# Kernel tuning notes

Measured on AMD Instinct MI355X. Metric: run time of the kernel, lower is better.

## Reference

```python
import jax, jax.numpy as jnp
import numpy as np

# Module constants (match init_kwargs / DCNv4 defaults)
N, C, H, W = 4, 256, 128, 128
G = 4                       # DCNv4 default group
KS = 3                      # kernel_size
K = KS * KS                 # 9 sampling points per group
Cg = C // G                 # channels per group
PAD_OFF = int(np.ceil(G * K * 3 / 8) * 8)  # 112, padded offset_mask dim
EPS = 1e-5                  # BatchNorm2d eps


def setup_inputs() -> dict:
    key = jax.random.key(0)
    ks = jax.random.split(key, 6)
    s = 0.05
    return {
        "x": jax.random.normal(ks[0], (N, C, H, W), jnp.float32),
        "conv_w": jax.random.normal(ks[1], (C, C, 1, 1), jnp.float32) * s,
        "bn1_gamma": jnp.ones((C,), jnp.float32),
        "bn1_beta": jnp.zeros((C,), jnp.float32),
        "bn1_mean": jnp.zeros((C,), jnp.float32),
        "bn1_var": jnp.ones((C,), jnp.float32),
        "value_w": jax.random.normal(ks[2], (C, C), jnp.float32) * s,
        "value_b": jnp.zeros((C,), jnp.float32),
        "offset_w": jax.random.normal(ks[3], (PAD_OFF, C), jnp.float32) * s,
        "offset_b": jnp.zeros((PAD_OFF,), jnp.float32),
        "out_w": jax.random.normal(ks[4], (C, C), jnp.float32) * s,
        "out_b": jnp.zeros((C,), jnp.float32),
        "bn2_gamma": jnp.ones((C,), jnp.float32),
        "bn2_beta": jnp.zeros((C,), jnp.float32),
        "bn2_mean": jnp.zeros((C,), jnp.float32),
        "bn2_var": jnp.ones((C,), jnp.float32),
    }


def _bilinear(v, lh, lw):
    """Bilinear sample v:(N,H,W,G,Cg) at float locs lh/lw:(N,H,W,G); zero outside."""
    n, h, w, g, c = v.shape
    h0 = jnp.floor(lh)
    w0 = jnp.floor(lw)
    dh = lh - h0
    dw = lw - w0
    h0i = h0.astype(jnp.int32)
    w0i = w0.astype(jnp.int32)
    vf = v.reshape(n, h * w, g, c)

    def gather(hh, ww):
        valid = (hh >= 0) & (hh < h) & (ww >= 0) & (ww < w)
        idx = jnp.clip(hh, 0, h - 1) * w + jnp.clip(ww, 0, w - 1)
        out = jnp.take_along_axis(vf, idx.reshape(n, h * w, g)[..., None], axis=1)
        return out.reshape(n, h, w, g, c) * valid[..., None].astype(v.dtype)

    w00 = (1 - dh) * (1 - dw)
    w01 = (1 - dh) * dw
    w10 = dh * (1 - dw)
    w11 = dh * dw
    return (gather(h0i, w0i) * w00[..., None]
            + gather(h0i, w0i + 1) * w01[..., None]
            + gather(h0i + 1, w0i) * w10[..., None]
            + gather(h0i + 1, w0i + 1) * w11[..., None])


def _bn(x_nchw, gamma, beta, mean, var):
    scale = (gamma / jnp.sqrt(var + EPS))[None, :, None, None]
    return x_nchw * scale + (beta - mean * gamma / jnp.sqrt(var + EPS))[None, :, None, None]


def reference(x, conv_w, bn1_gamma, bn1_beta, bn1_mean, bn1_var,
              value_w, value_b, offset_w, offset_b, out_w, out_b,
              bn2_gamma, bn2_beta, bn2_mean, bn2_var):
    n, _, h, w = x.shape
    # ---- Conv(c1,c2,k=1): 1x1 conv (no bias) + BN + SiLU ----
    y = jnp.einsum('nchw,oc->nohw', x, conv_w[:, :, 0, 0])
    y = jax.nn.silu(_bn(y, bn1_gamma, bn1_beta, bn1_mean, bn1_var))

    # ---- DCNv4 on (N, L, C) tokens ----
    t = y.transpose(0, 2, 3, 1)                      # (N,H,W,C)
    v = t @ value_w.T + value_b                      # value_proj
    om = t @ offset_w.T + offset_b                   # (N,H,W,112)
    om = om[..., : G * K * 3].reshape(n, h, w, G, K * 3)
    off = om[..., : 2 * K].reshape(n, h, w, G, K, 2) # (dx, dy) per point
    mask = om[..., 2 * K:]                           # (N,H,W,G,K), no softmax in v4
    v = v.reshape(n, h, w, G, Cg)

    hi = jnp.arange(h, dtype=jnp.float32)[None, :, None, None]
    wi = jnp.arange(w, dtype=jnp.float32)[None, None, :, None]
    out = jnp.zeros_like(v)
    for k in range(K):  # fixed small kernel loop (9 points)
        i, j = divmod(k, KS)
        lh = hi + (i - 1) + off[..., k, 1]           # stride=1, pad=1, dil=1
        lw = wi + (j - 1) + off[..., k, 0]           # offset_scale=1.0
        out = out + mask[..., k, None] * _bilinear(v, lh, lw)

    o = out.reshape(n, h, w, C) @ out_w.T + out_b    # output_proj
    o = o.transpose(0, 3, 1, 2)                      # back to NCHW

    # ---- final BN + SiLU ----
    return jax.nn.silu(_bn(o, bn2_gamma, bn2_beta, bn2_mean, bn2_var))
```

## Files before the change

kernel.cpp:

```cpp
#include <hip/hip_runtime.h>
#include <cstdint>

typedef unsigned short u16;
typedef unsigned int   u32;
typedef __attribute__((ext_vector_type(8))) __bf16 bf16x8;
typedef __attribute__((ext_vector_type(2))) float  f32x2;
typedef __attribute__((ext_vector_type(4))) float  f32x4;
typedef __attribute__((ext_vector_type(4))) u32    u32x4;

#define N_IMG 4
#define C_DIM 256
#define H_DIM 128
#define W_DIM 128
#define HW    (H_DIM * W_DIM)
#define M_TOT (N_IMG * HW)
#define CG    64
#define PADOFF 112
#define NCAT  368
#define EPSV  1e-5f

__device__ __forceinline__ u16 f2b(float f) {
  u32 u = __float_as_uint(f);
  u += 0x7fffu + ((u >> 16) & 1u);
  return (u16)(u >> 16);
}

__device__ __forceinline__ void async_cp16(const void* g, void* l) {
  __builtin_amdgcn_global_load_lds(
      (const __attribute__((address_space(1))) void*)g,
      (__attribute__((address_space(3))) void*)l, 16, 0, 0);
}

__global__ __launch_bounds__(256) void cast_all(
    const float* __restrict__ a0, u16* __restrict__ o0,
    const float* __restrict__ a1, u16* __restrict__ o1,
    const float* __restrict__ a2, u16* __restrict__ o2,
    const float* __restrict__ a3, u16* __restrict__ o3) {
  int i = blockIdx.x * 256 + threadIdx.x;
  const float* in; u16* out; int base;
  if (i < 16384)      { in = a0; out = o0; base = 0; }
  else if (i < 32768) { in = a1; out = o1; base = 16384; }
  else if (i < 39936) { in = a2; out = o2; base = 32768; }
  else                { in = a3; out = o3; base = 39936; }
  int j = i - base;
  f32x4 v = reinterpret_cast<const f32x4*>(in)[j];
  u32 lo = (u32)f2b(v[0]) | ((u32)f2b(v[1]) << 16);
  u32 hi = (u32)f2b(v[2]) | ((u32)f2b(v[3]) << 16);
  reinterpret_cast<u32*>(out)[2 * j]     = lo;
  reinterpret_cast<u32*>(out)[2 * j + 1] = hi;
}

__global__ __launch_bounds__(256, 2) void fused_proj(
    const float* __restrict__ X, const u16* __restrict__ Bc,
    const u16* __restrict__ Wcat,
    u16* __restrict__ Vv, float* __restrict__ Om,
    const float* __restrict__ vbias, const float* __restrict__ obias,
    const float* __restrict__ gamma, const float* __restrict__ beta,
    const float* __restrict__ mean, const float* __restrict__ var) {
  constexpr int BM = 128, BK = 32;
  __shared__ __align__(16) u16 T[BM * C_DIM];
  __shared__ __align__(16) u16 As[BM * BK];
  __shared__ __align__(16) u16 Bs[BM * BK];
  const int tid  = threadIdx.x;
  const int lane = tid & 63;
  const int wave = tid >> 6;
  const int quad = lane >> 4;
  const int l16  = lane & 15;
  const int bm = blockIdx.x * BM;
  const int wm = (wave & 1) * 64;
  const int wn = (wave >> 1) * 64;
  const int img = bm >> 14;
  const int hw0 = bm & (HW - 1);
  const int p2  = (tid & 63) * 2;
  const int hh  = tid >> 6;
  const float* xb = X + (size_t)img * C_DIM * HW + hw0 + p2;

  f32x4 acc0[4][4] = {};
  f32x4 acc1[4][4] = {};
  for (int ko = 0; ko < C_DIM; ko += BK) {
    float a0[8], a1[8];
#pragma unroll
    for (int j = 0; j < 8; ++j) {
      f32x2 fv = *reinterpret_cast<const f32x2*>(
          xb + (size_t)(ko + hh * 8 + j) * HW);
      a0[j] = fv.x; a1[j] = fv.y;
    }
    u32x4 w0, w1;
#pragma unroll
    for (int j = 0; j < 4; ++j) {
      w0[j] = (u32)f2b(a0[2 * j]) | ((u32)f2b(a0[2 * j + 1]) << 16);
      w1[j] = (u32)f2b(a1[2 * j]) | ((u32)f2b(a1[2 * j + 1]) << 16);
    }
    {
      u32x4* Ar = reinterpret_cast<u32x4*>(As);
      int sw = hh ^ ((p2 >> 1) & 3);
      Ar[p2 * 4 + sw]       = w0;
      Ar[(p2 + 1) * 4 + sw] = w1;
    }
#pragma unroll
    for (int it = 0; it < 2; ++it) {
      int chunk = it * 256 + tid;
      int r  = chunk >> 2;
      int kk = (chunk & 3) << 3;
      async_cp16(Bc + (size_t)r * C_DIM + (ko + kk),
                 Bs + (size_t)(it * 256 + wave * 64) * 8);
    }
    __syncthreads();
    const bf16x8* Apf = reinterpret_cast<const bf16x8*>(As);
    const bf16x8* Bpf = reinterpret_cast<const bf16x8*>(Bs);
    bf16x8 af[4];
#pragma unroll
    for (int mi = 0; mi < 4; ++mi) {
      int r = wm + mi * 16 + l16;
      af[mi] = Apf[r * 4 + (quad ^ ((r >> 1) & 3))];
    }
    {
      bf16x8 bfr[4];
#pragma unroll
      for (int ni = 0; ni < 4; ++ni)
        bfr[ni] = Bpf[(wn + ni * 16 + l16) * 4 + quad];
#pragma unroll
      for (int mi = 0; mi < 4; ++mi)
#pragma unroll
        for (int ni = 0; ni < 4; ++ni)
          acc0[mi][ni] = __builtin_amdgcn_mfma_f32_16x16x32_bf16(
              af[mi], bfr[ni], acc0[mi][ni], 0, 0, 0);
    }
    __syncthreads();
#pragma unroll
    for (int it = 0; it < 2; ++it) {
      int chunk = it * 256 + tid;
      int r  = chunk >> 2;
      int kk = (chunk & 3) << 3;
      async_cp16(Bc + (size_t)(128 + r) * C_DIM + (ko + kk),
                 Bs + (size_t)(it * 256 + wave * 64) * 8);
    }
    __syncthreads();
    {
      bf16x8 bfr[4];
#pragma unroll
      for (int ni = 0; ni < 4; ++ni)
        bfr[ni] = Bpf[(wn + ni * 16 + l16) * 4 + quad];
#pragma unroll
      for (int mi = 0; mi < 4; ++mi)
#pragma unroll
        for (int ni = 0; ni < 4; ++ni)
          acc1[mi][ni] = __builtin_amdgcn_mfma_f32_16x16x32_bf16(
              af[mi], bfr[ni], acc1[mi][ni], 0, 0, 0);
    }
    __syncthreads();
  }
  auto epi1 = [&](f32x4 (&acc)[4][4], int bn) {
#pragma unroll
    for (int ni = 0; ni < 4; ++ni) {
      int n = bn + wn + ni * 16 + l16;
      float sc = gamma[n] * rsqrtf(var[n] + EPSV);
      float sh = beta[n] - mean[n] * sc;
#pragma unroll
      for (int mi = 0; mi < 4; ++mi) {
        int row = wm + mi * 16 + quad * 4;
#pragma unroll
        for (int i = 0; i < 4; ++i) {
          float y = acc[mi][ni][i] * sc + sh;
          y = y / (1.f + __expf(-y));
          int rr = row + i;
          T[rr * C_DIM + (((n >> 3) ^ (rr & 15)) << 3) + (n & 7)] = f2b(y);
        }
      }
    }
  };
  epi1(acc0, 0);
  epi1(acc1, 128);
  __syncthreads();

  auto stage2 = [&](u16* buf, int n0, int ko) {
#pragma unroll
    for (int it = 0; it < 2; ++it) {
      int chunk = it * 256 + tid;
      int r  = chunk >> 2;
      int kk = (chunk & 3) << 3;
      int br = n0 + r; if (br >= NCAT) br = NCAT - 1;
      async_cp16(Wcat + (size_t)br * C_DIM + (ko + kk),
                 buf + (size_t)(it * 256 + wave * 64) * 8);
    }
  };
  for (int nc = 0; nc < 3; ++nc) {
    const int n0 = nc * 128;
    f32x4 acc[4][4] = {};
    stage2(As, n0, 0);
    for (int koi = 0; koi < 8; ++koi) {
      const u16* cur = (koi & 1) ? Bs : As;
      u16*       nxt = (koi & 1) ? As : Bs;
      if (koi < 7) {
        stage2(nxt, n0, (koi + 1) * BK);
        asm volatile("s_waitcnt vmcnt(2)" ::: "memory");
      } else {
        asm volatile("s_waitcnt vmcnt(0)" ::: "memory");
      }
      __builtin_amdgcn_sched_barrier(0);
      __builtin_amdgcn_s_barrier();
      __builtin_amdgcn_sched_barrier(0);
      const bf16x8* Bpf = reinterpret_cast<const bf16x8*>(cur);
      bf16x8 af[4], bfr[4];
#pragma unroll
      for (int mi = 0; mi < 4; ++mi) {
        int row = wm + mi * 16 + l16;
        int ch  = koi * 4 + quad;
        af[mi] = *reinterpret_cast<const bf16x8*>(
            &T[row * C_DIM + ((ch ^ (row & 15)) << 3)]);
      }
#pragma unroll
      for (int ni = 0; ni < 4; ++ni)
        bfr[ni] = Bpf[(wn + ni * 16 + l16) * 4 + quad];
#pragma unroll
      for (int mi = 0; mi < 4; ++mi)
#pragma unroll
        for (int ni = 0; ni < 4; ++ni)
          acc[mi][ni] = __builtin_amdgcn_mfma_f32_16x16x32_bf16(
              af[mi], bfr[ni], acc[mi][ni], 0, 0, 0);
      __builtin_amdgcn_sched_barrier(0);
      __builtin_amdgcn_s_barrier();
    }
#pragma unroll
    for (int ni = 0; ni < 4; ++ni) {
      int n = n0 + wn + ni * 16 + l16;
      if (n < C_DIM) {
        float sh = vbias[n];
#pragma unroll
        for (int mi = 0; mi < 4; ++mi) {
          int mrow = bm + wm + mi * 16 + quad * 4;
#pragma unroll
          for (int i = 0; i < 4; ++i)
            Vv[(size_t)(mrow + i) * C_DIM + n] = f2b(acc[mi][ni][i] + sh);
        }
      } else {
        int col = n - C_DIM;
        bool ok = col < PADOFF;
        float sh = ok ? obias[col] : 0.f;
#pragma unroll
        for (int mi = 0; mi < 4; ++mi) {
          int mrow = bm + wm + mi * 16 + quad * 4;
#pragma unroll
          for (int i = 0; i < 4; ++i)
            if (ok) Om[(size_t)(mrow + i) * PADOFF + col] = acc[mi][ni][i] + sh;
        }
      }
    }
  }
}

__global__ __launch_bounds__(256) void gemm_out(
    const u16* __restrict__ A, const u16* __restrict__ B,
    float* __restrict__ Cf,
    const float* __restrict__ bias,
    const float* __restrict__ gamma, const float* __restrict__ beta,
    const float* __restrict__ mean, const float* __restrict__ var) {
  constexpr int BM = 128, BK = 64;
  __shared__ __align__(16) u16 As[BM * BK];
  __shared__ __align__(16) u16 Bs[BM * BK];
  const int tid  = threadIdx.x;
  const int lane = tid & 63;
  const int wave = tid >> 6;
  const int quad = lane >> 4;
  const int l16  = lane & 15;
  const int bm = blockIdx.x * BM;
  const int bn = blockIdx.y * BM;
  const int wm = (wave & 1) * 64;
  const int wn = (wave >> 1) * 64;

  f32x4 acc[4][4] = {};

  for (int ko = 0; ko < C_DIM; ko += BK) {
#pragma unroll
    for (int it = 0; it < 4; ++it) {
      int chunk = it * 256 + tid;
      int r  = chunk >> 3;
      int j  = chunk & 7;
      int kk = (j ^ (r & 7)) << 3;
      async_cp16(A + (size_t)(bm + r) * C_DIM + (ko + kk),
                 As + (size_t)(it * 256 + wave * 64) * 8);
      async_cp16(B + (size_t)(bn + r) * C_DIM + (ko + kk),
                 Bs + (size_t)(it * 256 + wave * 64) * 8);
    }
    __syncthreads();
    const bf16x8* Ap = reinterpret_cast<const bf16x8*>(As);
    const bf16x8* Bp = reinterpret_cast<const bf16x8*>(Bs);
#pragma unroll
    for (int ks = 0; ks < 2; ++ks) {
      bf16x8 af[4], bfr[4];
#pragma unroll
      for (int mi = 0; mi < 4; ++mi) {
        int row = wm + mi * 16 + l16;
        af[mi] = Ap[row * 8 + ((ks * 4 + quad) ^ (row & 7))];
      }
#pragma unroll
      for (int ni = 0; ni < 4; ++ni) {
        int row = wn + ni * 16 + l16;
        bfr[ni] = Bp[row * 8 + ((ks * 4 + quad) ^ (row & 7))];
      }
#pragma unroll
      for (int mi = 0; mi < 4; ++mi)
#pragma unroll
        for (int ni = 0; ni < 4; ++ni)
          acc[mi][ni] = __builtin_amdgcn_mfma_f32_16x16x32_bf16(
              af[mi], bfr[ni], acc[mi][ni], 0, 0, 0);
    }
    __syncthreads();
  }

#pragma unroll
  for (int ni = 0; ni < 4; ++ni) {
    int n = bn + wn + ni * 16 + l16;
    float sc = gamma[n] * rsqrtf(var[n] + EPSV);
    float sh = beta[n] - mean[n] * sc + bias[n] * sc;
#pragma unroll
    for (int mi = 0; mi < 4; ++mi) {
      int mrow = bm + wm + mi * 16 + quad * 4;
      int img = mrow >> 14;
      int hw  = mrow & (HW - 1);
      f32x4 y;
#pragma unroll
      for (int i = 0; i < 4; ++i) {
        float z = acc[mi][ni][i] * sc + sh;
        y[i] = z / (1.f + __expf(-z));
      }
      *reinterpret_cast<f32x4*>(
          Cf + (size_t)img * C_DIM * HW + (size_t)n * HW + hw) = y;
    }
  }
}

__global__ __launch_bounds__(256) void dcn_sample(
    const u16* __restrict__ v, const float* __restrict__ om,
    u16* __restrict__ outp) {
  __shared__ float sm[16 * PADOFF];
  const int tid = threadIdx.x;
  const int bid = blockIdx.x;
  const int cpx = gridDim.x >> 3;
  const int wg  = (bid & 7) * cpx + (bid >> 3);
  const int m0  = wg * 16;
  {
    const float* src = om + (size_t)m0 * PADOFF;
#pragma unroll
    for (int i = 0; i < 7; ++i) sm[tid + i * 256] = src[tid + i * 256];
  }
  __syncthreads();
  const int c4 = tid & 3;
  const int g  = (tid >> 2) & 3;
  const int pl = tid >> 4;
  const int m  = m0 + pl;
  const int n  = m >> 14;
  const int hw = m & (HW - 1);
  const int h = hw >> 7, w = hw & 127;
  const float* p = sm + pl * PADOFF + g * 27;
  const u16* vb = v + (size_t)n * HW * C_DIM + g * CG + c4 * 16;
  float acc[16] = {};
#pragma unroll
  for (int k = 0; k < 9; ++k) {
    const int di = k / 3 - 1, dj = k % 3 - 1;
    float ox = p[2 * k], oy = p[2 * k + 1], mk = p[18 + k];
    float lh = (float)(h + di) + oy;
    float lw = (float)(w + dj) + ox;
    float fh = floorf(lh), fw = floorf(lw);
    float dh = lh - fh, dw = lw - fw;
    int h0 = (int)fh, w0 = (int)fw;
    float wy0 = (1.f - dh) * mk, wy1 = dh * mk;
    float wx0 = 1.f - dw, wx1 = dw;
    bool okw0 = (u32)w0 < (u32)W_DIM;
    bool okw1 = (u32)(w0 + 1) < (u32)W_DIM;
    int w0c = min(max(w0, 0), W_DIM - 1);
    int w1c = min(max(w0 + 1, 0), W_DIM - 1);
#pragma unroll
    for (int cy = 0; cy < 2; ++cy) {
      int hh = h0 + cy;
      bool okh = (u32)hh < (u32)H_DIM;
      int hc = min(max(hh, 0), H_DIM - 1);
      const u16* rowp = vb + (size_t)(hc << 7) * C_DIM;
      const u16* qA = rowp + (size_t)w0c * C_DIM;
      const u16* qB = rowp + (size_t)w1c * C_DIM;
      u32x4 a0 = *reinterpret_cast<const u32x4*>(qA);
      u32x4 a1 = *reinterpret_cast<const u32x4*>(qA + 8);
      u32x4 b0 = *reinterpret_cast<const u32x4*>(qB);
      u32x4 b1 = *reinterpret_cast<const u32x4*>(qB + 8);
      float wyc = (cy == 0) ? wy0 : wy1;
      float wtA = (okh && okw0) ? wyc * wx0 : 0.f;
      float wtB = (okh && okw1) ? wyc * wx1 : 0.f;
      u32 wp;
      asm("v_cvt_pk_bf16_f32 %0, %1, %2" : "=v"(wp) : "v"(wtA), "v"(wtB));
#pragma unroll
      for (int j = 0; j < 4; ++j) {
        u32 lo0 = __builtin_amdgcn_perm(a0[j], b0[j], 0x01000504u);
        u32 hi0 = __builtin_amdgcn_perm(a0[j], b0[j], 0x03020706u);
        u32 lo1 = __builtin_amdgcn_perm(a1[j], b1[j], 0x01000504u);
        u32 hi1 = __builtin_amdgcn_perm(a1[j], b1[j], 0x03020706u);
        asm("v_dot2_f32_bf16 %0, %1, %2, %3"
            : "=v"(acc[2 * j]) : "v"(lo0), "v"(wp), "v"(acc[2 * j]));
        asm("v_dot2_f32_bf16 %0, %1, %2, %3"
            : "=v"(acc[2 * j + 1]) : "v"(hi0), "v"(wp), "v"(acc[2 * j + 1]));
        asm("v_dot2_f32_bf16 %0, %1, %2, %3"
            : "=v"(acc[8 + 2 * j]) : "v"(lo1), "v"(wp), "v"(acc[8 + 2 * j]));
        asm("v_dot2_f32_bf16 %0, %1, %2, %3"
            : "=v"(acc[8 + 2 * j + 1]) : "v"(hi1), "v"(wp), "v"(acc[8 + 2 * j + 1]));
      }
    }
  }
  u32x4 r0, r1;
#pragma unroll
  for (int j = 0; j < 4; ++j) {
    u32 pa, pb;
    asm("v_cvt_pk_bf16_f32 %0, %1, %2"
        : "=v"(pa) : "v"(acc[2 * j]), "v"(acc[2 * j + 1]));
    asm("v_cvt_pk_bf16_f32 %0, %1, %2"
        : "=v"(pb) : "v"(acc[8 + 2 * j]), "v"(acc[8 + 2 * j + 1]));
    r0[j] = pa; r1[j] = pb;
  }
  u16* o = outp + (size_t)m * C_DIM + g * CG + c4 * 16;
  *reinterpret_cast<u32x4*>(o)     = r0;
  *reinterpret_cast<u32x4*>(o + 8) = r1;
}

extern "C" void kernel_launch(void* const* d_in, const int* in_sizes, int n_in,
                              void* d_out, int out_size, void* d_ws, size_t ws_size,
                              hipStream_t stream) {
  const float* x        = (const float*)d_in[0];
  const float* conv_w   = (const float*)d_in[1];
  const float* bn1_g    = (const float*)d_in[2];
  const float* bn1_b    = (const float*)d_in[3];
  const float* bn1_m    = (const float*)d_in[4];
  const float* bn1_v    = (const float*)d_in[5];
  const float* value_w  = (const float*)d_in[6];
  const float* value_b  = (const float*)d_in[7];
  const float* offset_w = (const float*)d_in[8];
  const float* offset_b = (const float*)d_in[9];
  const float* out_w    = (const float*)d_in[10];
  const float* out_b    = (const float*)d_in[11];
  const float* bn2_g    = (const float*)d_in[12];
  const float* bn2_b    = (const float*)d_in[13];
  const float* bn2_m    = (const float*)d_in[14];
  const float* bn2_v    = (const float*)d_in[15];

  char* ws = (char*)d_ws;
  u16*   vv   = (u16*)(ws);
  float* om   = (float*)(ws + 33554432);
  u16*   dcn  = (u16*)(ws + 67108864);
  u16*   wc   = (u16*)(ws + 100663296);
  u16*   wcat = (u16*)(ws + 100794368);
  u16*   wout = (u16*)(ws + 100982784);
  float* outp = (float*)d_out;

  cast_all<<<220, 256, 0, stream>>>(conv_w, wc, value_w, wcat,
                                    offset_w, wcat + 65536, out_w, wout);

  fused_proj<<<dim3(M_TOT / 128), 256, 0, stream>>>(
      x, wc, wcat, vv, om, value_b, offset_b,
      bn1_g, bn1_b, bn1_m, bn1_v);
  dcn_sample<<<dim3(M_TOT / 16), 256, 0, stream>>>(vv, om, dcn);
  gemm_out<<<dim3(M_TOT / 128, 2), 256, 0, stream>>>(
      dcn, wout, outp, out_b, bn2_g, bn2_b, bn2_m, bn2_v);
}
```

Before: 260.7 us.

## Double-buffer output-projection GEMM K-loop with BK=32 async prefetch

The output-projection GEMM now uses two shared-memory buffers with BK=32 and prefetches the next K slice via async copies while MFMAs run on the current one. Explicit vmcnt waits and s_barrier calls replace the two __syncthreads per iteration. The XOR swizzle on the LDS layout is dropped, which may add bank conflicts on fragment reads. The loop gets twice as many iterations, each with less work.

```diff
diff --git a/kernel.cpp b/kernel.cpp
--- a/kernel.cpp
+++ b/kernel.cpp
@@ -255,9 +255,9 @@
     const float* __restrict__ bias,
     const float* __restrict__ gamma, const float* __restrict__ beta,
     const float* __restrict__ mean, const float* __restrict__ var) {
-  constexpr int BM = 128, BK = 64;
-  __shared__ __align__(16) u16 As[BM * BK];
-  __shared__ __align__(16) u16 Bs[BM * BK];
+  constexpr int BM = 128, BK = 32;
+  __shared__ __align__(16) u16 As[2][BM * BK];
+  __shared__ __align__(16) u16 Bs[2][BM * BK];
   const int tid  = threadIdx.x;
   const int lane = tid & 63;
   const int wave = tid >> 6;
@@ -268,44 +268,48 @@
   const int wm = (wave & 1) * 64;
   const int wn = (wave >> 1) * 64;
 
+  auto stage = [&](int buf, int ko) {
+#pragma unroll
+    for (int it = 0; it < 2; ++it) {
+      int chunk = it * 256 + tid;
+      int r  = chunk >> 2;
+      int kk = (chunk & 3) << 3;
+      async_cp16(A + (size_t)(bm + r) * C_DIM + (ko + kk),
+                 &As[buf][(it * 256 + wave * 64) * 8]);
+      async_cp16(B + (size_t)(bn + r) * C_DIM + (ko + kk),
+                 &Bs[buf][(it * 256 + wave * 64) * 8]);
+    }
+  };
+
   f32x4 acc[4][4] = {};
 
-  for (int ko = 0; ko < C_DIM; ko += BK) {
-#pragma unroll
-    for (int it = 0; it < 4; ++it) {
-      int chunk = it * 256 + tid;
-      int r  = chunk >> 3;
-      int j  = chunk & 7;
-      int kk = (j ^ (r & 7)) << 3;
-      async_cp16(A + (size_t)(bm + r) * C_DIM + (ko + kk),
-                 As + (size_t)(it * 256 + wave * 64) * 8);
-      async_cp16(B + (size_t)(bn + r) * C_DIM + (ko + kk),
-                 Bs + (size_t)(it * 256 + wave * 64) * 8);
-    }
-    __syncthreads();
-    const bf16x8* Ap = reinterpret_cast<const bf16x8*>(As);
-    const bf16x8* Bp = reinterpret_cast<const bf16x8*>(Bs);
-#pragma unroll
-    for (int ks = 0; ks < 2; ++ks) {
-      bf16x8 af[4], bfr[4];
-#pragma unroll
-      for (int mi = 0; mi < 4; ++mi) {
-        int row = wm + mi * 16 + l16;
-        af[mi] = Ap[row * 8 + ((ks * 4 + quad) ^ (row & 7))];
-      }
-#pragma unroll
-      for (int ni = 0; ni < 4; ++ni) {
-        int row = wn + ni * 16 + l16;
-        bfr[ni] = Bp[row * 8 + ((ks * 4 + quad) ^ (row & 7))];
-      }
-#pragma unroll
-      for (int mi = 0; mi < 4; ++mi)
-#pragma unroll
-        for (int ni = 0; ni < 4; ++ni)
-          acc[mi][ni] = __builtin_amdgcn_mfma_f32_16x16x32_bf16(
-              af[mi], bfr[ni], acc[mi][ni], 0, 0, 0);
-    }
-    __syncthreads();
+  stage(0, 0);
+  for (int t = 0; t < 8; ++t) {
+    const int cur = t & 1;
+    if (t < 7) {
+      stage(cur ^ 1, (t + 1) * BK);
+      asm volatile("s_waitcnt vmcnt(4)" ::: "memory");
+    } else {
+      asm volatile("s_waitcnt vmcnt(0)" ::: "memory");
+    }
+    __builtin_amdgcn_sched_barrier(0);
+    __builtin_amdgcn_s_barrier();
+    __builtin_amdgcn_sched_barrier(0);
+    const bf16x8* Ap = reinterpret_cast<const bf16x8*>(As[cur]);
+    const bf16x8* Bp = reinterpret_cast<const bf16x8*>(Bs[cur]);
+    bf16x8 af[4], bfr[4];
+#pragma unroll
+    for (int mi = 0; mi < 4; ++mi) af[mi] = Ap[(wm + mi * 16 + l16) * 4 + quad];
+#pragma unroll
+    for (int ni = 0; ni < 4; ++ni) bfr[ni] = Bp[(wn + ni * 16 + l16) * 4 + quad];
+#pragma unroll
+    for (int mi = 0; mi < 4; ++mi)
+#pragma unroll
+      for (int ni = 0; ni < 4; ++ni)
+        acc[mi][ni] = __builtin_amdgcn_mfma_f32_16x16x32_bf16(
+            af[mi], bfr[ni], acc[mi][ni], 0, 0, 0);
+    __builtin_amdgcn_sched_barrier(0);
+    __builtin_amdgcn_s_barrier();
   }
 
 #pragma unroll
```

Result: faster. 252.0 us (-3.4%).
